# Performance work log

Hardware: AMD Instinct MI355X
Metric: run time of the kernel (lower is better)

Reference implementation:

```python
import jax, jax.numpy as jnp
import numpy as np

B, S, HIDDEN = 2, 4096, 4096
NUM_HEADS = 32
QK_NOPE = 128
QK_ROPE = 64
QK_HEAD = QK_NOPE + QK_ROPE
KV_LORA = 512
Q_LORA = 1536


def setup_inputs() -> dict:
    key = jax.random.key(0)
    k1, k2, k3, k4, k5, k6 = jax.random.split(key, 6)
    x = jax.random.normal(k1, (B, S, HIDDEN), dtype=jnp.float32)
    cos = jax.random.uniform(k2, (B, S, QK_ROPE), dtype=jnp.float32)
    sin = jax.random.uniform(k3, (B, S, QK_ROPE), dtype=jnp.float32)
    # Linear weights, torch layout [out, in]
    Wqa = jax.random.normal(k4, (Q_LORA, HIDDEN), dtype=jnp.float32) * 0.02
    Wqb = jax.random.normal(k5, (NUM_HEADS * QK_HEAD, Q_LORA), dtype=jnp.float32) * 0.02
    Wkva = jax.random.normal(k6, (KV_LORA + QK_ROPE, HIDDEN), dtype=jnp.float32) * 0.02
    return {"x": x, "cos": cos, "sin": sin, "Wqa": Wqa, "Wqb": Wqb, "Wkva": Wkva}


def _rotate_half(t):
    d = t.shape[-1] // 2
    return jnp.concatenate([-t[..., d:], t[..., :d]], axis=-1)


def reference(x, cos, sin, Wqa, Wqb, Wkva):
    b, s, _ = x.shape
    # low-rank Q: x -> q_lora -> heads*(nope+rope)
    q = jnp.einsum('bsh,rh->bsr', x, Wqa)
    q = jnp.einsum('bsr,or->bso', q, Wqb).reshape(b, s, NUM_HEADS, QK_HEAD)
    q_nope = q[..., :QK_NOPE]
    q_pe = q[..., QK_NOPE:]
    # KV down-projection with MQA rope part
    kv = jnp.einsum('bsh,oh->bso', x, Wkva)
    compressed_kv = kv[..., :KV_LORA]                         # [b,s,kv_lora]
    k_pe = kv[..., KV_LORA:].reshape(b, s, 1, QK_ROPE)
    # NeoX explicit RoPE, unsqueeze_dim=2
    c = cos[:, :, None, :]
    sn = sin[:, :, None, :]
    q_pe_rot = q_pe * c + _rotate_half(q_pe) * sn
    k_pe_rot = k_pe * c + _rotate_half(k_pe) * sn
    q_out = jnp.concatenate([q_nope, q_pe_rot], axis=-1).reshape(b, s, -1)
    k_out = k_pe_rot.reshape(b, s, QK_ROPE)
    return jnp.concatenate([q_out, k_out, compressed_kv], axis=-1)
```

## Files before the change

### kernel.cpp

```cpp
#include <hip/hip_runtime.h>
#include <hip/hip_bf16.h>
#include <stdint.h>

typedef __bf16 bf16x8 __attribute__((ext_vector_type(8)));
typedef float f32x4 __attribute__((ext_vector_type(4)));
typedef float fvec4 __attribute__((ext_vector_type(4)));
typedef unsigned short usvec4 __attribute__((ext_vector_type(4)));
typedef unsigned int ui32x4 __attribute__((ext_vector_type(4)));

#define AS3 __attribute__((address_space(3)))
#define AS1 __attribute__((address_space(1)))

static __device__ __forceinline__ unsigned short f2bf(float f) {
  unsigned int u = __float_as_uint(f);
  u += 0x7FFF + ((u >> 16) & 1);
  return (unsigned short)(u >> 16);
}


extern "C" __global__ void cvt_bf16_kernel(const float* __restrict__ src,
                                           unsigned short* __restrict__ dst,
                                           long n4) {
  long i = (long)blockIdx.x * blockDim.x + threadIdx.x;
  const long stride = (long)gridDim.x * blockDim.x;
  for (; i < n4; i += stride) {
    const fvec4 v = __builtin_nontemporal_load(&((const fvec4*)src)[i]);
    usvec4 o;
    o.x = f2bf(v.x); o.y = f2bf(v.y); o.z = f2bf(v.z); o.w = f2bf(v.w);
    ((usvec4*)dst)[i] = o;
  }
}

extern "C" __global__ void cvt_pad_kernel(const float* __restrict__ src,
                                          unsigned short* __restrict__ dst,
                                          long nsrc4, long ntot4) {
  long i = (long)blockIdx.x * blockDim.x + threadIdx.x;
  const long stride = (long)gridDim.x * blockDim.x;
  for (; i < ntot4; i += stride) {
    usvec4 o = {0, 0, 0, 0};
    if (i < nsrc4) {
      const fvec4 v = __builtin_nontemporal_load(&((const fvec4*)src)[i]);
      o.x = f2bf(v.x); o.y = f2bf(v.y); o.z = f2bf(v.z); o.w = f2bf(v.w);
    }
    ((usvec4*)dst)[i] = o;
  }
}


#define VMW(N) asm volatile("s_waitcnt vmcnt(" #N ")" ::: "memory")
#define BAR() do { __builtin_amdgcn_s_barrier(); \
                   __builtin_amdgcn_sched_barrier(0); } while (0)
#define LGKM0() do { asm volatile("s_waitcnt lgkmcnt(0)" ::: "memory"); \
                     __builtin_amdgcn_sched_barrier(0); } while (0)

template <int MODE>
__global__ __launch_bounds__(512, 2)
void mla_gemm(const __hip_bfloat16* __restrict__ A0p,
              const __hip_bfloat16* __restrict__ B0p, int K0,
              const __hip_bfloat16* __restrict__ A1p,
              const __hip_bfloat16* __restrict__ B1p,
              unsigned short* __restrict__ qlora,
              const float* __restrict__ cosp,
              const float* __restrict__ sinp,
              float* __restrict__ out) {
  extern __shared__ __align__(128) char lds[];
  const int tid = threadIdx.x;
  const int lane = tid & 63;
  const int w = tid >> 6;
  const int wm = w >> 2, wn = w & 3;
  const int l15 = lane & 15, lhi = lane >> 4;
  const int srow8 = lane >> 3;
  const int swzc = ((lane & 7) ^ srow8) * 8;

  const __hip_bfloat16* Aptr;
  const __hip_bfloat16* Bptr;
  int K, bm, bn;
  bool isA2 = false;
  if constexpr (MODE == 0) {
    const int swz = ((int)blockIdx.x & 7) * 32 + ((int)blockIdx.x >> 3);
    bm = swz >> 3; bn = swz & 7;
    Aptr = A0p; Bptr = B0p; K = K0;
  } else {
    const int bid = (int)blockIdx.x;
    if (bid < 32) {
      isA2 = true; bm = bid; bn = 8; Aptr = A1p; Bptr = B1p; K = 4096;
    } else {
      const int b2 = bid - 32;
      const int swz = (b2 & 7) * 96 + (b2 >> 3);
      bm = swz / 24; bn = swz - bm * 24;
      Aptr = A0p; Bptr = B0p; K = K0;
    }
  }
  const long brow = (long)bm * 256;
  const int bcol = bn * 256;

  const __hip_bfloat16* aSt = Aptr + (brow + w * 16 + srow8) * (long)K + swzc;
  const __hip_bfloat16* bSt = Bptr + ((long)bcol + srow8) * (long)K + swzc;
  const int wj0 = w * 16, wj1 = w * 16 + 8;
  const int cb_j0 = (2 * (wj0 >> 5)) * 32 + (wj0 & 31);
  const int cb_j1 = (2 * (wj1 >> 5)) * 32 + (wj1 & 31);
  const int ldsWj = w * 2048;

  const int aRdRow = (wm * 64 + l15) * 128;
  const int bRdRow = (wn * 32 + l15) * 128;
  const int ck0 = (lhi ^ (l15 & 7)) * 16;

  f32x4 acc[8][4] = {};
  bf16x8 aF[4][2];
  bf16x8 bF[2][2][2];

  const int T = K >> 6;

  auto stage = [&](int u, int kt) {
    const int b = kt & 1;
    if (u < 2) {
      const int off = b * 32768 + u * 16384 + ldsWj;
      __builtin_amdgcn_global_load_lds((AS1 void*)(aSt + (long)(u * 128) * K + kt * 64),
                                       (AS3 void*)(lds + off), 16, 0, 0);
      __builtin_amdgcn_global_load_lds((AS1 void*)(aSt + (long)(u * 128 + 8) * K + kt * 64),
                                       (AS3 void*)(lds + off + 1024), 16, 0, 0);
    } else {
      const int h = u - 2;
      const int off = 65536 + b * 32768 + h * 16384 + ldsWj;
      __builtin_amdgcn_global_load_lds((AS1 void*)(bSt + (long)(cb_j0 + h * 32) * K + kt * 64),
                                       (AS3 void*)(lds + off), 16, 0, 0);
      __builtin_amdgcn_global_load_lds((AS1 void*)(bSt + (long)(cb_j1 + h * 32) * K + kt * 64),
                                       (AS3 void*)(lds + off + 1024), 16, 0, 0);
    }
  };
  auto readA = [&](int qh, int b) {
    const int base = b * 32768 + qh * 16384 + aRdRow;
    #pragma unroll
    for (int fr = 0; fr < 4; ++fr) {
      aF[fr][0] = *(const bf16x8*)(lds + base + fr * 2048 + ck0);
      aF[fr][1] = *(const bf16x8*)(lds + base + fr * 2048 + (ck0 ^ 64));
    }
  };
  auto readB = [&](int c, int b) {
    const int base = 65536 + b * 32768 + c * 16384 + bRdRow;
    #pragma unroll
    for (int fq = 0; fq < 2; ++fq) {
      bF[c][fq][0] = *(const bf16x8*)(lds + base + fq * 2048 + ck0);
      bF[c][fq][1] = *(const bf16x8*)(lds + base + fq * 2048 + (ck0 ^ 64));
    }
  };
  auto mmac = [&](int qh, int c) {
    __builtin_amdgcn_s_setprio(1);
    #pragma unroll
    for (int fr = 0; fr < 4; ++fr)
      #pragma unroll
      for (int fq = 0; fq < 2; ++fq) {
        acc[qh * 4 + fr][c * 2 + fq] = __builtin_amdgcn_mfma_f32_16x16x32_bf16(
            aF[fr][0], bF[c][fq][0], acc[qh * 4 + fr][c * 2 + fq], 0, 0, 0);
        acc[qh * 4 + fr][c * 2 + fq] = __builtin_amdgcn_mfma_f32_16x16x32_bf16(
            aF[fr][1], bF[c][fq][1], acc[qh * 4 + fr][c * 2 + fq], 0, 0, 0);
      }
    __builtin_amdgcn_s_setprio(0);
  };

  stage(0, 0); stage(2, 0); stage(3, 0); stage(1, 0);
  stage(0, 1); stage(2, 1); stage(3, 1); stage(1, 1);
  VMW(12);
  BAR();

  for (int t = 0; t < T - 2; ++t) {
    const int b = t & 1;
    readA(0, b); readB(0, b); if (t) stage(1, t + 1);
    VMW(10); BAR(); LGKM0(); mmac(0, 0);
    readB(1, b);
    VMW(8); BAR(); LGKM0(); mmac(0, 1);
    readA(1, b); stage(0, t + 2); stage(2, t + 2);
    BAR(); LGKM0(); mmac(1, 1);
    stage(3, t + 2);
    VMW(10); BAR(); mmac(1, 0);
  }
  {
    const int b = (T - 2) & 1;
    readA(0, b); readB(0, b); stage(1, T - 1);
    VMW(10); BAR(); LGKM0(); mmac(0, 0);
    readB(1, b);
    VMW(8); BAR(); LGKM0(); mmac(0, 1);
    readA(1, b);
    BAR(); LGKM0(); mmac(1, 1);
    VMW(4); BAR(); mmac(1, 0);
  }
  {
    const int b = (T - 1) & 1;
    readA(0, b); readB(0, b);
    VMW(2); BAR(); LGKM0(); mmac(0, 0);
    readB(1, b);
    VMW(0); BAR(); LGKM0(); mmac(0, 1);
    readA(1, b);
    BAR(); LGKM0(); mmac(1, 1);
    BAR(); mmac(1, 0);
  }

  const int wcol = bcol + wn * 64;
  const long rbase = brow + wm * 64;
  char* eplds = lds + w * 4096;

  auto storeTileF32 = [&](int i8, float* dst, bool rope) {
    #pragma unroll
    for (int j = 0; j < 4; ++j)
      #pragma unroll
      for (int r = 0; r < 4; ++r) {
        float v = acc[i8][j][r];
        if (rope) {
          const long row = rbase + (i8 >> 2) * 128 + (i8 & 3) * 16 + lhi * 4 + r;
          const int d = (j >> 1) * 32 + (j & 1) * 16 + l15;
          const float rot = (j < 2) ? -acc[i8][j + 2][r] : acc[i8][j - 2][r];
          v = v * cosp[row * 64 + d] + rot * sinp[row * 64 + d];
        }
        *(float*)(eplds + (lhi * 4 + r) * 256 + ((j >> 1) * 32 + (j & 1) * 16 + l15) * 4) = v;
      }
    asm volatile("s_waitcnt lgkmcnt(0)" ::: "memory");
    #pragma unroll
    for (int t = 0; t < 4; ++t) {
      const int r16 = t * 4 + (lane >> 4);
      const f32x4 v = *(const f32x4*)(eplds + r16 * 256 + (lane & 15) * 16);
      const long row = rbase + (i8 >> 2) * 128 + (i8 & 3) * 16 + r16;
      __builtin_nontemporal_store(v, (f32x4*)(dst + row * 6720 + (lane & 15) * 4));
    }
  };
  auto storeTileBf16 = [&](int i8) {
    #pragma unroll
    for (int j = 0; j < 4; ++j)
      #pragma unroll
      for (int r = 0; r < 4; ++r)
        *(unsigned short*)(eplds + (lhi * 4 + r) * 128 +
                           ((j >> 1) * 32 + (j & 1) * 16 + l15) * 2) = f2bf(acc[i8][j][r]);
    asm volatile("s_waitcnt lgkmcnt(0)" ::: "memory");
    #pragma unroll
    for (int t = 0; t < 2; ++t) {
      const int r16 = t * 8 + (lane >> 3);
      const ui32x4 v = *(const ui32x4*)(eplds + r16 * 128 + (lane & 7) * 16);
      const long row = rbase + (i8 >> 2) * 128 + (i8 & 3) * 16 + r16;
      *(ui32x4*)((char*)qlora + (row * 1536 + wcol) * 2 + (lane & 7) * 16) = v;
    }
  };

  if constexpr (MODE == 0) {
    if (wcol < 1536) {
      #pragma unroll
      for (int i8 = 0; i8 < 8; ++i8) storeTileBf16(i8);
    } else {
      #pragma unroll
      for (int i8 = 0; i8 < 8; ++i8) storeTileF32(i8, out + wcol + 4672, false);
    }
  } else {
    if (isA2) {
      if (wn == 0) {
        #pragma unroll
        for (int i8 = 0; i8 < 8; ++i8) storeTileF32(i8, out + 6144, true);
      }
    } else if ((wcol % 192) != 128) {
      #pragma unroll
      for (int i8 = 0; i8 < 8; ++i8) storeTileF32(i8, out + wcol, false);
    } else {
      #pragma unroll
      for (int i8 = 0; i8 < 8; ++i8) storeTileF32(i8, out + wcol, true);
    }
  }
}


extern "C" void kernel_launch(void* const* d_in, const int* in_sizes, int n_in,
                              void* d_out, int out_size, void* d_ws, size_t ws_size,
                              hipStream_t stream) {
  const float* x    = (const float*)d_in[0];
  const float* cosp = (const float*)d_in[1];
  const float* sinp = (const float*)d_in[2];
  const float* Wqa  = (const float*)d_in[3];
  const float* Wqb  = (const float*)d_in[4];
  const float* Wkva = (const float*)d_in[5];
  float* out = (float*)d_out;

  char* ws = (char*)d_ws;
  __hip_bfloat16* xb  = (__hip_bfloat16*)ws;
  __hip_bfloat16* w1  = (__hip_bfloat16*)(ws + 67108864L);
  __hip_bfloat16* wqb = (__hip_bfloat16*)(ws + 67108864L + 17825792L);
  unsigned short* ql  = (unsigned short*)(ws + 67108864L + 17825792L + 18874368L);

  cvt_bf16_kernel<<<2048, 256, 0, stream>>>(x,   (unsigned short*)xb,  8192L * 4096 / 4);
  cvt_bf16_kernel<<<1024, 256, 0, stream>>>(Wqa, (unsigned short*)w1,  1536L * 4096 / 4);
  cvt_pad_kernel<<<640, 256, 0, stream>>>(Wkva, (unsigned short*)(w1 + 1536L * 4096),
                                          576L * 4096 / 4, 640L * 4096 / 4);
  cvt_bf16_kernel<<<1024, 256, 0, stream>>>(Wqb, (unsigned short*)wqb, 6144L * 1536 / 4);

  (void)hipFuncSetAttribute((const void*)&mla_gemm<0>,
                            hipFuncAttributeMaxDynamicSharedMemorySize, 131072);
  (void)hipFuncSetAttribute((const void*)&mla_gemm<1>,
                            hipFuncAttributeMaxDynamicSharedMemorySize, 131072);

  mla_gemm<0><<<dim3(256), 512, 131072, stream>>>(xb, w1, 4096, nullptr, nullptr,
                                                  ql, cosp, sinp, out);
  mla_gemm<1><<<dim3(800), 512, 131072, stream>>>((const __hip_bfloat16*)ql, wqb, 1536,
                                                  xb, w1, ql, cosp, sinp, out);
}
```

Measured before the change: 341.1 us.

## Replace second GEMM with dedicated 256x128 triple-buffered kernel using direct-to-LDS loads

The second projection (q_lora to heads plus the k_pe tile) moves from the shared 256x256 templated kernel into a new kernel with 256x128 tiles and K-step 32. It triple-buffers through global_load_lds and allows higher occupancy (launch bounds 512,4 with 72KB LDS). The grid grows to 1568 blocks, which is meant to improve load balance and tail behaviour on the short K=1536 GEMM. The trade-off is smaller tiles with less operand reuse and more barrier and loop overhead per FLOP.

```diff
diff --git a/kernel.cpp b/kernel.cpp
--- a/kernel.cpp
+++ b/kernel.cpp
@@ -46,19 +46,17 @@
   }
 }
 
-
 #define VMW(N) asm volatile("s_waitcnt vmcnt(" #N ")" ::: "memory")
 #define BAR() do { __builtin_amdgcn_s_barrier(); \
                    __builtin_amdgcn_sched_barrier(0); } while (0)
 #define LGKM0() do { asm volatile("s_waitcnt lgkmcnt(0)" ::: "memory"); \
                      __builtin_amdgcn_sched_barrier(0); } while (0)
 
+
 template <int MODE>
 __global__ __launch_bounds__(512, 2)
 void mla_gemm(const __hip_bfloat16* __restrict__ A0p,
               const __hip_bfloat16* __restrict__ B0p, int K0,
-              const __hip_bfloat16* __restrict__ A1p,
-              const __hip_bfloat16* __restrict__ B1p,
               unsigned short* __restrict__ qlora,
               const float* __restrict__ cosp,
               const float* __restrict__ sinp,
@@ -72,25 +70,11 @@
   const int srow8 = lane >> 3;
   const int swzc = ((lane & 7) ^ srow8) * 8;
 
-  const __hip_bfloat16* Aptr;
-  const __hip_bfloat16* Bptr;
-  int K, bm, bn;
-  bool isA2 = false;
-  if constexpr (MODE == 0) {
-    const int swz = ((int)blockIdx.x & 7) * 32 + ((int)blockIdx.x >> 3);
-    bm = swz >> 3; bn = swz & 7;
-    Aptr = A0p; Bptr = B0p; K = K0;
-  } else {
-    const int bid = (int)blockIdx.x;
-    if (bid < 32) {
-      isA2 = true; bm = bid; bn = 8; Aptr = A1p; Bptr = B1p; K = 4096;
-    } else {
-      const int b2 = bid - 32;
-      const int swz = (b2 & 7) * 96 + (b2 >> 3);
-      bm = swz / 24; bn = swz - bm * 24;
-      Aptr = A0p; Bptr = B0p; K = K0;
-    }
-  }
+  const int swz = ((int)blockIdx.x & 7) * 32 + ((int)blockIdx.x >> 3);
+  const int bm = swz >> 3, bn = swz & 7;
+  const __hip_bfloat16* Aptr = A0p;
+  const __hip_bfloat16* Bptr = B0p;
+  const int K = K0;
   const long brow = (long)bm * 256;
   const int bcol = bn * 256;
 
@@ -199,20 +183,13 @@
   const long rbase = brow + wm * 64;
   char* eplds = lds + w * 4096;
 
-  auto storeTileF32 = [&](int i8, float* dst, bool rope) {
+  auto storeTileF32 = [&](int i8, float* dst) {
     #pragma unroll
     for (int j = 0; j < 4; ++j)
       #pragma unroll
-      for (int r = 0; r < 4; ++r) {
-        float v = acc[i8][j][r];
-        if (rope) {
-          const long row = rbase + (i8 >> 2) * 128 + (i8 & 3) * 16 + lhi * 4 + r;
-          const int d = (j >> 1) * 32 + (j & 1) * 16 + l15;
-          const float rot = (j < 2) ? -acc[i8][j + 2][r] : acc[i8][j - 2][r];
-          v = v * cosp[row * 64 + d] + rot * sinp[row * 64 + d];
-        }
-        *(float*)(eplds + (lhi * 4 + r) * 256 + ((j >> 1) * 32 + (j & 1) * 16 + l15) * 4) = v;
-      }
+      for (int r = 0; r < 4; ++r)
+        *(float*)(eplds + (lhi * 4 + r) * 256 + ((j >> 1) * 32 + (j & 1) * 16 + l15) * 4) =
+            acc[i8][j][r];
     asm volatile("s_waitcnt lgkmcnt(0)" ::: "memory");
     #pragma unroll
     for (int t = 0; t < 4; ++t) {
@@ -239,27 +216,144 @@
     }
   };
 
-  if constexpr (MODE == 0) {
-    if (wcol < 1536) {
-      #pragma unroll
-      for (int i8 = 0; i8 < 8; ++i8) storeTileBf16(i8);
-    } else {
-      #pragma unroll
-      for (int i8 = 0; i8 < 8; ++i8) storeTileF32(i8, out + wcol + 4672, false);
-    }
+  if (wcol < 1536) {
+    #pragma unroll
+    for (int i8 = 0; i8 < 8; ++i8) storeTileBf16(i8);
   } else {
-    if (isA2) {
-      if (wn == 0) {
-        #pragma unroll
-        for (int i8 = 0; i8 < 8; ++i8) storeTileF32(i8, out + 6144, true);
+    #pragma unroll
+    for (int i8 = 0; i8 < 8; ++i8) storeTileF32(i8, out + wcol + 4672);
+  }
+}
+
+
+__global__ __launch_bounds__(512, 4)
+void mla_gemm2(const __hip_bfloat16* __restrict__ Aq,
+               const __hip_bfloat16* __restrict__ Bq,
+               const __hip_bfloat16* __restrict__ Ak,
+               const __hip_bfloat16* __restrict__ Bk,
+               const float* __restrict__ cosp,
+               const float* __restrict__ sinp,
+               float* __restrict__ out) {
+  extern __shared__ __align__(128) char lds[];
+  const int tid = threadIdx.x;
+  const int lane = tid & 63;
+  const int w = tid >> 6;
+  const int wm = w >> 1, wn = w & 1;
+  const int l15 = lane & 15, lhi = lane >> 4;
+  const int srow = lane >> 2;
+  const int sslot = (lane & 3) ^ ((lane >> 3) & 3);
+
+  const __hip_bfloat16* Ap;
+  const __hip_bfloat16* Bp;
+  int K, bm, bn;
+  bool kpe;
+  const int bid = (int)blockIdx.x;
+  if (bid < 32) {
+    kpe = true; bm = bid; bn = 0; Ap = Ak; Bp = Bk; K = 4096;
+  } else {
+    kpe = false;
+    const int b2 = bid - 32;
+    const int swz = (b2 & 7) * 192 + (b2 >> 3);
+    bm = swz / 48; bn = swz - bm * 48;
+    Ap = Aq; Bp = Bq; K = 1536;
+  }
+  const long brow = (long)bm * 256;
+  const int bcol = bn * 128;
+
+  const __hip_bfloat16* aSt = Ap + (brow + w * 16 + srow) * (long)K + sslot * 8;
+  const __hip_bfloat16* bSt = Bp + ((long)bcol + w * 16 + srow) * (long)K + sslot * 8;
+
+  const int kslot = (lhi ^ ((l15 >> 1) & 3)) * 16;
+  const int aRd = (wm * 64 + l15) * 64 + kslot;
+  const int bRd = 16384 + (wn * 64 + l15) * 64 + kslot;
+
+  f32x4 acc[4][4] = {};
+  const int T = K >> 5;
+
+  auto stage = [&](int kt, int buf) {
+    const int bo = buf * 24576;
+    __builtin_amdgcn_global_load_lds((AS1 void*)(aSt + (long)kt * 32),
+                                     (AS3 void*)(lds + bo + w * 1024), 16, 0, 0);
+    __builtin_amdgcn_global_load_lds((AS1 void*)(aSt + 128L * K + (long)kt * 32),
+                                     (AS3 void*)(lds + bo + 8192 + w * 1024), 16, 0, 0);
+    __builtin_amdgcn_global_load_lds((AS1 void*)(bSt + (long)kt * 32),
+                                     (AS3 void*)(lds + bo + 16384 + w * 1024), 16, 0, 0);
+  };
+
+  stage(0, 0); stage(1, 1);
+  VMW(3);
+  BAR();
+
+  int cur = 0;
+  for (int t = 0; t < T; ++t) {
+    const int bo = cur * 24576;
+    bf16x8 aF[4], bF[4];
+    #pragma unroll
+    for (int f = 0; f < 4; ++f)
+      aF[f] = *(const bf16x8*)(lds + bo + aRd + f * 1024);
+    #pragma unroll
+    for (int f = 0; f < 4; ++f)
+      bF[f] = *(const bf16x8*)(lds + bo + bRd + f * 1024);
+    if (t + 2 < T) {
+      int nx = cur + 2; if (nx >= 3) nx -= 3;
+      stage(t + 2, nx);
+      VMW(3);
+    } else if (t + 2 == T) {
+      VMW(0);
+    }
+    LGKM0();
+    if (t < T - 1) BAR();
+    __builtin_amdgcn_s_setprio(1);
+    #pragma unroll
+    for (int fr = 0; fr < 4; ++fr)
+      #pragma unroll
+      for (int fc = 0; fc < 4; ++fc)
+        acc[fr][fc] = __builtin_amdgcn_mfma_f32_16x16x32_bf16(
+            aF[fr], bF[fc], acc[fr][fc], 0, 0, 0);
+    __builtin_amdgcn_s_setprio(0);
+    cur = cur + 1; if (cur == 3) cur = 0;
+  }
+
+  const int wcol = bcol + wn * 64;
+  const long rbase = brow + wm * 64;
+  char* eplds = lds + w * 4096;
+
+  auto storeT = [&](int fr, int colBase, bool rope) {
+    #pragma unroll
+    for (int fc = 0; fc < 4; ++fc)
+      #pragma unroll
+      for (int r = 0; r < 4; ++r) {
+        float v = acc[fr][fc][r];
+        if (rope) {
+          const long row = rbase + fr * 16 + lhi * 4 + r;
+          const int d = fc * 16 + l15;
+          const float rot = (fc < 2) ? -acc[fr][fc + 2][r] : acc[fr][fc - 2][r];
+          v = v * cosp[row * 64 + d] + rot * sinp[row * 64 + d];
+        }
+        *(float*)(eplds + (lhi * 4 + r) * 256 + (fc * 16 + l15) * 4) = v;
       }
-    } else if ((wcol % 192) != 128) {
-      #pragma unroll
-      for (int i8 = 0; i8 < 8; ++i8) storeTileF32(i8, out + wcol, false);
-    } else {
-      #pragma unroll
-      for (int i8 = 0; i8 < 8; ++i8) storeTileF32(i8, out + wcol, true);
-    }
+    asm volatile("s_waitcnt lgkmcnt(0)" ::: "memory");
+    #pragma unroll
+    for (int tt = 0; tt < 4; ++tt) {
+      const int r16 = tt * 4 + (lane >> 4);
+      const f32x4 vv = *(const f32x4*)(eplds + r16 * 256 + (lane & 15) * 16);
+      const long row = rbase + fr * 16 + r16;
+      __builtin_nontemporal_store(vv,
+          (f32x4*)(out + row * 6720 + colBase + (lane & 15) * 4));
+    }
+  };
+
+  if (kpe) {
+    if (wn == 0) {
+      #pragma unroll
+      for (int fr = 0; fr < 4; ++fr) storeT(fr, 6144, true);
+    }
+  } else if ((wcol % 192) == 128) {
+    #pragma unroll
+    for (int fr = 0; fr < 4; ++fr) storeT(fr, wcol, true);
+  } else {
+    #pragma unroll
+    for (int fr = 0; fr < 4; ++fr) storeT(fr, wcol, false);
   }
 }
 
@@ -289,11 +383,11 @@
 
   (void)hipFuncSetAttribute((const void*)&mla_gemm<0>,
                             hipFuncAttributeMaxDynamicSharedMemorySize, 131072);
-  (void)hipFuncSetAttribute((const void*)&mla_gemm<1>,
-                            hipFuncAttributeMaxDynamicSharedMemorySize, 131072);
-
-  mla_gemm<0><<<dim3(256), 512, 131072, stream>>>(xb, w1, 4096, nullptr, nullptr,
-                                                  ql, cosp, sinp, out);
-  mla_gemm<1><<<dim3(800), 512, 131072, stream>>>((const __hip_bfloat16*)ql, wqb, 1536,
-                                                  xb, w1, ql, cosp, sinp, out);
-}
+  (void)hipFuncSetAttribute((const void*)&mla_gemm2,
+                            hipFuncAttributeMaxDynamicSharedMemorySize, 73728);
+
+  mla_gemm<0><<<dim3(256), 512, 131072, stream>>>(xb, w1, 4096, ql, cosp, sinp, out);
+  mla_gemm2<<<dim3(1568), 512, 73728, stream>>>((const __hip_bfloat16*)ql, wqb,
+                                                xb, w1 + 2048L * 4096,
+                                                cosp, sinp, out);
+}
```

Result: slower. 362.9 us (+6.4%).

## Split-K the k_pe rope tile into partials with a separate RoPE reduce kernel

Applied to the files above, without the earlier changes.

The 32 long-K (4096) blocks that compute the k_pe rope columns in the second GEMM launch are replaced by 256 split-K blocks, each covering a 512-wide K slice. Their fp32 partials go to a workspace buffer, and a new reduce kernel sums the 8 slices and applies RoPE before writing the output. This is meant to remove the tail where a few long blocks run after the short-K q blocks finish. In exchange it adds partial-buffer traffic, uncoalesced scalar stores, and one extra kernel launch.

```diff
diff --git a/kernel.cpp b/kernel.cpp
--- a/kernel.cpp
+++ b/kernel.cpp
@@ -47,6 +47,25 @@
 }
 
 
+extern "C" __global__ void kpe_reduce_kernel(const float* __restrict__ part,
+                                             const float* __restrict__ cosp,
+                                             const float* __restrict__ sinp,
+                                             float* __restrict__ out) {
+  const int idx = (int)blockIdx.x * 256 + threadIdx.x;
+  const int row = idx >> 6, d = idx & 63;
+  const int pidx = (idx - d) + ((d < 32) ? d + 32 : d - 32);
+  float s = 0.f, sp = 0.f;
+  #pragma unroll
+  for (int ks = 0; ks < 8; ++ks) {
+    s  += part[(long)ks * 524288 + idx];
+    sp += part[(long)ks * 524288 + pidx];
+  }
+  const float rot = (d < 32) ? -sp : sp;
+  out[(long)row * 6720 + 6144 + d] =
+      s * cosp[(long)row * 64 + d] + rot * sinp[(long)row * 64 + d];
+}
+
+
 #define VMW(N) asm volatile("s_waitcnt vmcnt(" #N ")" ::: "memory")
 #define BAR() do { __builtin_amdgcn_s_barrier(); \
                    __builtin_amdgcn_sched_barrier(0); } while (0)
@@ -59,6 +78,7 @@
               const __hip_bfloat16* __restrict__ B0p, int K0,
               const __hip_bfloat16* __restrict__ A1p,
               const __hip_bfloat16* __restrict__ B1p,
+              float* __restrict__ kpart,
               unsigned short* __restrict__ qlora,
               const float* __restrict__ cosp,
               const float* __restrict__ sinp,
@@ -74,28 +94,30 @@
 
   const __hip_bfloat16* Aptr;
   const __hip_bfloat16* Bptr;
-  int K, bm, bn;
+  int K, bm, bn, T, koff = 0, ks = 0;
   bool isA2 = false;
   if constexpr (MODE == 0) {
     const int swz = ((int)blockIdx.x & 7) * 32 + ((int)blockIdx.x >> 3);
     bm = swz >> 3; bn = swz & 7;
-    Aptr = A0p; Bptr = B0p; K = K0;
+    Aptr = A0p; Bptr = B0p; K = K0; T = K0 >> 6;
   } else {
     const int bid = (int)blockIdx.x;
-    if (bid < 32) {
-      isA2 = true; bm = bid; bn = 8; Aptr = A1p; Bptr = B1p; K = 4096;
+    if (bid >= 768) {
+      isA2 = true;
+      bm = (bid - 768) >> 3; bn = 8; ks = (bid - 768) & 7;
+      Aptr = A1p; Bptr = B1p; K = 4096; T = 8; koff = ks * 512;
     } else {
-      const int b2 = bid - 32;
+      const int b2 = bid;
       const int swz = (b2 & 7) * 96 + (b2 >> 3);
       bm = swz / 24; bn = swz - bm * 24;
-      Aptr = A0p; Bptr = B0p; K = K0;
+      Aptr = A0p; Bptr = B0p; K = K0; T = K0 >> 6;
     }
   }
   const long brow = (long)bm * 256;
   const int bcol = bn * 256;
 
-  const __hip_bfloat16* aSt = Aptr + (brow + w * 16 + srow8) * (long)K + swzc;
-  const __hip_bfloat16* bSt = Bptr + ((long)bcol + srow8) * (long)K + swzc;
+  const __hip_bfloat16* aSt = Aptr + (brow + w * 16 + srow8) * (long)K + swzc + koff;
+  const __hip_bfloat16* bSt = Bptr + ((long)bcol + srow8) * (long)K + swzc + koff;
   const int wj0 = w * 16, wj1 = w * 16 + 8;
   const int cb_j0 = (2 * (wj0 >> 5)) * 32 + (wj0 & 31);
   const int cb_j1 = (2 * (wj1 >> 5)) * 32 + (wj1 & 31);
@@ -108,8 +130,6 @@
   f32x4 acc[8][4] = {};
   bf16x8 aF[4][2];
   bf16x8 bF[2][2][2];
-
-  const int T = K >> 6;
 
   auto stage = [&](int u, int kt) {
     const int b = kt & 1;
@@ -250,8 +270,17 @@
   } else {
     if (isA2) {
       if (wn == 0) {
+        float* pp = kpart + (long)ks * 524288;
         #pragma unroll
-        for (int i8 = 0; i8 < 8; ++i8) storeTileF32(i8, out + 6144, true);
+        for (int i8 = 0; i8 < 8; ++i8)
+          #pragma unroll
+          for (int j = 0; j < 4; ++j)
+            #pragma unroll
+            for (int r = 0; r < 4; ++r) {
+              const long row = rbase + (i8 >> 2) * 128 + (i8 & 3) * 16 + lhi * 4 + r;
+              const int d = (j >> 1) * 32 + (j & 1) * 16 + l15;
+              pp[row * 64 + d] = acc[i8][j][r];
+            }
       }
     } else if ((wcol % 192) != 128) {
       #pragma unroll
@@ -280,6 +309,7 @@
   __hip_bfloat16* w1  = (__hip_bfloat16*)(ws + 67108864L);
   __hip_bfloat16* wqb = (__hip_bfloat16*)(ws + 67108864L + 17825792L);
   unsigned short* ql  = (unsigned short*)(ws + 67108864L + 17825792L + 18874368L);
+  float* kpart        = (float*)(ws + 67108864L + 17825792L + 18874368L + 25165824L);
 
   cvt_bf16_kernel<<<2048, 256, 0, stream>>>(x,   (unsigned short*)xb,  8192L * 4096 / 4);
   cvt_bf16_kernel<<<1024, 256, 0, stream>>>(Wqa, (unsigned short*)w1,  1536L * 4096 / 4);
@@ -293,7 +323,8 @@
                             hipFuncAttributeMaxDynamicSharedMemorySize, 131072);
 
   mla_gemm<0><<<dim3(256), 512, 131072, stream>>>(xb, w1, 4096, nullptr, nullptr,
-                                                  ql, cosp, sinp, out);
-  mla_gemm<1><<<dim3(800), 512, 131072, stream>>>((const __hip_bfloat16*)ql, wqb, 1536,
-                                                  xb, w1, ql, cosp, sinp, out);
-}
+                                                  nullptr, ql, cosp, sinp, out);
+  mla_gemm<1><<<dim3(1024), 512, 131072, stream>>>((const __hip_bfloat16*)ql, wqb, 1536,
+                                                   xb, w1, kpart, ql, cosp, sinp, out);
+  kpe_reduce_kernel<<<dim3(2048), 256, 0, stream>>>(kpart, cosp, sinp, out);
+}
```

After: 331.6 us. -2.8%, faster.
